# Kernel tuning notes

Hardware: AMD Instinct MI355X
Metric: run time of the kernel (lower is better)

The kernel has to match this reference:

```python
import jax, jax.numpy as jnp
import numpy as np

B, T, H = 16, 512, 384   # batch, phoneme length, hidden
F, K = 384, 3            # filter size, kernel size
DMAX = 8                 # max per-token duration
L = T * DMAX             # static max expanded length (original uses real_len.max())


def conv1d_same(x, w, b):
    # x: [B, T, Cin], w: [Cout, Cin, K] (torch OIW layout), padding = K//2 both sides
    y = jax.lax.conv_general_dilated(
        x.transpose(0, 2, 1), w, window_strides=(1,),
        padding=[(K // 2, K // 2)], dimension_numbers=('NCW', 'OIW', 'NCW'))
    return y.transpose(0, 2, 1) + b


def layer_norm(x, g, b, eps=1e-5):
    mu = jnp.mean(x, axis=-1, keepdims=True)
    var = jnp.mean(jnp.square(x - mu), axis=-1, keepdims=True)
    return (x - mu) * jax.lax.rsqrt(var + eps) * g + b


def setup_inputs() -> dict:
    key = jax.random.key(0)
    ks = jax.random.split(key, 10)
    x = jax.random.normal(ks[0], (B, T, H), dtype=jnp.float32)
    # log-durations whose exp().round() gives integers in [1, DMAX]
    dur = jax.random.randint(ks[1], (B, T), 1, DMAX + 1)
    true_durations = jnp.log(dur.astype(jnp.float32))
    s1 = 1.0 / np.sqrt(H * K)
    s2 = 1.0 / np.sqrt(F * K)
    s3 = 1.0 / np.sqrt(F)
    return {
        'x': x,
        'true_durations': true_durations,
        'conv1_w': jax.random.uniform(ks[2], (F, H, K), jnp.float32, -s1, s1),
        'conv1_b': jnp.zeros((F,), jnp.float32),
        'ln1_g': jnp.ones((F,), jnp.float32),
        'ln1_b': jnp.zeros((F,), jnp.float32),
        'conv2_w': jax.random.uniform(ks[3], (F, F, K), jnp.float32, -s2, s2),
        'conv2_b': jnp.zeros((F,), jnp.float32),
        'ln2_g': jnp.ones((F,), jnp.float32),
        'ln2_b': jnp.zeros((F,), jnp.float32),
        'lin_w': jax.random.uniform(ks[4], (F, 1), jnp.float32, -s3, s3),
        'lin_b': jnp.zeros((1,), jnp.float32),
    }


def reference(x, true_durations, conv1_w, conv1_b, ln1_g, ln1_b,
              conv2_w, conv2_b, ln2_g, ln2_b, lin_w, lin_b):
    # duration predictor net (dropout in eval mode = identity)
    h = conv1d_same(x, conv1_w, conv1_b)
    h = jax.nn.gelu(layer_norm(h, ln1_g, ln1_b), approximate=False)
    h = conv1d_same(h, conv2_w, conv2_b)
    h = jax.nn.gelu(layer_norm(h, ln2_g, ln2_b), approximate=False)
    length = jax.nn.relu(h @ lin_w + lin_b)[..., 0]  # [B, T]

    # length regulation with ground-truth durations (detached ints in original)
    dur = jnp.round(jnp.exp(true_durations)).astype(jnp.int32)  # [B, T]
    ends = jnp.cumsum(dur, axis=1)          # [B, T]
    starts = ends - dur                     # [B, T]
    k = jnp.arange(L)                       # [L]
    # binary alignment: A[b,t,l] = 1 iff starts[b,t] <= l < ends[b,t]
    A = ((k >= starts[..., None]) & (k < ends[..., None])).astype(x.dtype)  # [B,T,L]
    out = jnp.einsum('bth,btl->blh', x, A)  # = (x^T @ A)^T, [B, L, H]
    return out, length
```

## Files before the change

kernel.cpp:

```cpp
#include <hip/hip_runtime.h>
#include <stdint.h>

typedef unsigned short u16;
typedef unsigned int   u32;

#define B_    16
#define T_    512
#define H_    384
#define F_    384
#define DMAX_ 8
#define L_    4096
#define KD    1152
#define M_    8192

typedef __bf16 bf16x8 __attribute__((ext_vector_type(8)));
typedef float  f32x4  __attribute__((ext_vector_type(4)));

typedef __attribute__((address_space(1))) u32 gu32;
typedef __attribute__((address_space(3))) u32 lu32;

__device__ __forceinline__ void dma16(const void* g, void* l) {
    __builtin_amdgcn_global_load_lds((gu32*)(uintptr_t)g, (lu32*)(u32)(uintptr_t)l, 16, 0, 0);
}

__device__ __forceinline__ u16 f2b(float f) {
    union { float f; u32 i; } v; v.f = f;
    u32 x = v.i;
    return (u16)((x + 0x7fffu + ((x >> 16) & 1u)) >> 16);
}

__global__ void k_prep(const float* __restrict__ td, const float* __restrict__ w1,
                       const float* __restrict__ w2, const float* __restrict__ x,
                       int* __restrict__ tmap, u16* __restrict__ Wp1,
                       u16* __restrict__ Wp2, u16* __restrict__ xb,
                       u16* __restrict__ zp) {
    int blk = blockIdx.x, tid = threadIdx.x;
    if (blk < 16) {
        __shared__ int s[T_];
        int b = blk, t = tid;
        int d = (int)roundf(expf(td[b * T_ + t]));
        if (d < 0) d = 0; if (d > DMAX_) d = DMAX_;
        int v = d;
        s[t] = v;
        __syncthreads();
        for (int off = 1; off < T_; off <<= 1) {
            int add = (t >= off) ? s[t - off] : 0;
            __syncthreads();
            v += add;
            s[t] = v;
            __syncthreads();
        }
        int end = v, start = end - d;
        for (int i = start; i < end; ++i) tmap[b * L_ + i] = t;
        int total = s[T_ - 1];
        for (int l = total + t; l < L_; l += T_) tmap[b * L_ + l] = -1;
    } else if (blk == 16) {
        zp[tid] = 0;
    } else if (blk < 17 + 1728) {
        int j = (blk - 17) * 512 + tid;
        const int n = F_ * H_ * 3;
        const float* src = (j < n) ? w1 : w2;
        u16* dst         = (j < n) ? Wp1 : Wp2;
        int jj = (j < n) ? j : j - n;
        int f = jj / (H_ * 3);
        int rem = jj % (H_ * 3);
        int c = rem / 3, kk = rem % 3;
        dst[f * KD + kk * H_ + c] = f2b(src[jj]);
    } else {
        int v = (blk - 1745) * 512 + tid;
        float4 f = *(const float4*)(x + (size_t)v * 4);
        u16 o[4] = { f2b(f.x), f2b(f.y), f2b(f.z), f2b(f.w) };
        *(uint2*)(xb + (size_t)v * 4) = *(uint2*)o;
    }
}

__global__ void k_expand(const float* __restrict__ x, const int* __restrict__ tmap,
                         float* __restrict__ out) {
    int v = blockIdx.x * blockDim.x + threadIdx.x;
    if (v >= B_ * L_ * 96) return;
    int row = v / 96, c4 = v % 96;
    int b = row >> 12;
    int t = tmap[row];
    uint4 val = make_uint4(0u, 0u, 0u, 0u);
    if (t >= 0) val = *(const uint4*)(x + (size_t)((b << 9) + t) * H_ + c4 * 4);
    *(uint4*)(out + (size_t)row * H_ + c4 * 4) = val;
}

#define CH_ 3328

__device__ __forceinline__ void gemm_core(u16* smem, const u16* __restrict__ src,
                                          const u16* __restrict__ Wp,
                                          const u16* __restrict__ zp,
                                          int m0, int tid, f32x4 acc[2][3]) {
    int w = tid >> 6, lane = tid & 63;
    int quad = lane >> 4, l16 = lane & 15;

    const u16* bbase[6];
    int bdst[6];
    #pragma unroll
    for (int p = 0; p < 6; ++p) {
        int bc = p * 512 + tid;
        int rowB = bc >> 3;
        int qlB = (bc & 7) ^ (rowB & 7);
        bbase[p] = Wp + (size_t)rowB * KD + qlB * 8;
        bdst[p] = bc;
    }
    const u16* abase[3];
    int adst = 3072 + tid;
    {
        int rowA = (tid & 255) >> 3;
        int qlA = (tid & 7) ^ (rowA & 7);
        int arow = m0 + rowA;
        int bB = arow >> 9, tt = arow & 511;
        #pragma unroll
        for (int kk = 0; kk < 3; ++kk) {
            int ts = tt + kk - 1;
            abase[kk] = (ts >= 0 && ts < T_) ? (src + (size_t)((bB << 9) + ts) * H_ + qlA * 8)
                                             : (zp + qlA * 8);
        }
    }

    int aoff[2][2], boff[3][2];
    #pragma unroll
    for (int i = 0; i < 2; ++i)
        #pragma unroll
        for (int kv = 0; kv < 2; ++kv) {
            int row = i * 16 + l16;
            aoff[i][kv] = (3072 + ((row << 3) | ((kv * 4 + quad) ^ (row & 7)))) * 8;
        }
    #pragma unroll
    for (int j = 0; j < 3; ++j)
        #pragma unroll
        for (int kv = 0; kv < 2; ++kv) {
            int row = w * 48 + j * 16 + l16;
            boff[j][kv] = (((row << 3) | ((kv * 4 + quad) ^ (row & 7)))) * 8;
        }

    #pragma unroll
    for (int i = 0; i < 2; ++i)
        #pragma unroll
        for (int j = 0; j < 3; ++j)
            acc[i][j] = f32x4{0.f, 0.f, 0.f, 0.f};

    {
        u16* base = smem;
        #pragma unroll
        for (int p = 0; p < 6; ++p) dma16(bbase[p], base + (size_t)bdst[p] * 8);
        if (tid < 256) dma16(abase[0], base + (size_t)adst * 8);
    }

    int kk1 = 0, s61 = 0;
    for (int s = 0; s < 18; ++s) {
        __syncthreads();
        if (s < 17) {
            if (++s61 == 6) { s61 = 0; ++kk1; }
            int koff = (s + 1) * 64;
            u16* base = smem + (size_t)(((s + 1) & 1) ? CH_ : 0) * 8;
            #pragma unroll
            for (int p = 0; p < 6; ++p) dma16(bbase[p] + koff, base + (size_t)bdst[p] * 8);
            if (tid < 256) dma16(abase[kk1] + s61 * 64, base + (size_t)adst * 8);
        }
        const u16* rb = smem + (size_t)((s & 1) ? CH_ : 0) * 8;
        #pragma unroll
        for (int kv = 0; kv < 2; ++kv) {
            bf16x8 af0 = *(const bf16x8*)(rb + aoff[0][kv]);
            bf16x8 af1 = *(const bf16x8*)(rb + aoff[1][kv]);
            #pragma unroll
            for (int j = 0; j < 3; ++j) {
                bf16x8 bf = *(const bf16x8*)(rb + boff[j][kv]);
                acc[0][j] = __builtin_amdgcn_mfma_f32_16x16x32_bf16(af0, bf, acc[0][j], 0, 0, 0);
                acc[1][j] = __builtin_amdgcn_mfma_f32_16x16x32_bf16(af1, bf, acc[1][j], 0, 0, 0);
            }
        }
    }
    __syncthreads();
}

__launch_bounds__(512, 2)
__global__ void k_gemm1(const u16* __restrict__ xb, const u16* __restrict__ Wp,
                        const float* __restrict__ bias, const float* __restrict__ g,
                        const float* __restrict__ beta, u16* __restrict__ G,
                        const u16* __restrict__ zp) {
    __shared__ u16 smem[2 * CH_ * 8];
    int tid = threadIdx.x;
    int w = tid >> 6, lane = tid & 63;
    int quad = lane >> 4, l16 = lane & 15;
    int m0 = blockIdx.x * 32;

    f32x4 acc[2][3];
    gemm_core(smem, xb, Wp, zp, m0, tid, acc);

    float bcol[3], gcol[3], becol[3];
    #pragma unroll
    for (int j = 0; j < 3; ++j) {
        int col = w * 48 + j * 16 + l16;
        bcol[j] = bias[col]; gcol[j] = g[col]; becol[j] = beta[col];
    }
    float* sb  = (float*)smem;
    float* s2b = (float*)smem + 256;
    #pragma unroll
    for (int i = 0; i < 2; ++i)
        #pragma unroll
        for (int r = 0; r < 4; ++r) {
            float s = 0.f, s2 = 0.f;
            #pragma unroll
            for (int j = 0; j < 3; ++j) {
                float y = acc[i][j][r] + bcol[j];
                s += y; s2 += y * y;
            }
            #pragma unroll
            for (int off = 8; off; off >>= 1) { s += __shfl_down(s, off); s2 += __shfl_down(s2, off); }
            if (l16 == 0) {
                int rl = i * 16 + quad * 4 + r;
                sb[w * 32 + rl] = s; s2b[w * 32 + rl] = s2;
            }
        }
    __syncthreads();
    #pragma unroll
    for (int i = 0; i < 2; ++i)
        #pragma unroll
        for (int r = 0; r < 4; ++r) {
            int rl = i * 16 + quad * 4 + r;
            float S = 0.f, S2 = 0.f;
            #pragma unroll
            for (int w2 = 0; w2 < 8; ++w2) { S += sb[w2 * 32 + rl]; S2 += s2b[w2 * 32 + rl]; }
            float mean = S * (1.f / F_);
            float var  = S2 * (1.f / F_) - mean * mean;
            float rstd = rsqrtf(var + 1e-5f);
            #pragma unroll
            for (int j = 0; j < 3; ++j) {
                int col = w * 48 + j * 16 + l16;
                float y  = (acc[i][j][r] + bcol[j] - mean) * rstd * gcol[j] + becol[j];
                float gl = 0.5f * y * (1.f + erff(y * 0.70710678118654752f));
                G[(size_t)(m0 + rl) * F_ + col] = f2b(gl);
            }
        }
}

__launch_bounds__(512, 2)
__global__ void k_gemm2(const u16* __restrict__ G, const u16* __restrict__ Wp,
                        const float* __restrict__ bias, const float* __restrict__ g,
                        const float* __restrict__ beta, const float* __restrict__ lw,
                        const float* __restrict__ lb, float* __restrict__ out1,
                        const u16* __restrict__ zp) {
    __shared__ u16 smem[2 * CH_ * 8];
    int tid = threadIdx.x;
    int w = tid >> 6, lane = tid & 63;
    int quad = lane >> 4, l16 = lane & 15;
    int m0 = blockIdx.x * 32;

    f32x4 acc[2][3];
    gemm_core(smem, G, Wp, zp, m0, tid, acc);

    float bcol[3], gcol[3], becol[3], lwcol[3];
    #pragma unroll
    for (int j = 0; j < 3; ++j) {
        int col = w * 48 + j * 16 + l16;
        bcol[j] = bias[col]; gcol[j] = g[col]; becol[j] = beta[col]; lwcol[j] = lw[col];
    }
    float* sb  = (float*)smem;
    float* s2b = (float*)smem + 256;
    float* db  = (float*)smem + 512;
    #pragma unroll
    for (int i = 0; i < 2; ++i)
        #pragma unroll
        for (int r = 0; r < 4; ++r) {
            float s = 0.f, s2 = 0.f;
            #pragma unroll
            for (int j = 0; j < 3; ++j) {
                float y = acc[i][j][r] + bcol[j];
                s += y; s2 += y * y;
            }
            #pragma unroll
            for (int off = 8; off; off >>= 1) { s += __shfl_down(s, off); s2 += __shfl_down(s2, off); }
            if (l16 == 0) {
                int rl = i * 16 + quad * 4 + r;
                sb[w * 32 + rl] = s; s2b[w * 32 + rl] = s2;
            }
        }
    __syncthreads();
    #pragma unroll
    for (int i = 0; i < 2; ++i)
        #pragma unroll
        for (int r = 0; r < 4; ++r) {
            int rl = i * 16 + quad * 4 + r;
            float S = 0.f, S2 = 0.f;
            #pragma unroll
            for (int w2 = 0; w2 < 8; ++w2) { S += sb[w2 * 32 + rl]; S2 += s2b[w2 * 32 + rl]; }
            float mean = S * (1.f / F_);
            float var  = S2 * (1.f / F_) - mean * mean;
            float rstd = rsqrtf(var + 1e-5f);
            float dot = 0.f;
            #pragma unroll
            for (int j = 0; j < 3; ++j) {
                float y  = (acc[i][j][r] + bcol[j] - mean) * rstd * gcol[j] + becol[j];
                float gl = 0.5f * y * (1.f + erff(y * 0.70710678118654752f));
                dot += gl * lwcol[j];
            }
            #pragma unroll
            for (int off = 8; off; off >>= 1) dot += __shfl_down(dot, off);
            if (l16 == 0) db[w * 32 + rl] = dot;
        }
    __syncthreads();
    if (tid < 32) {
        float d = lb[0];
        #pragma unroll
        for (int w2 = 0; w2 < 8; ++w2) d += db[w2 * 32 + tid];
        out1[m0 + tid] = fmaxf(d, 0.f);
    }
}

extern "C" void kernel_launch(void* const* d_in, const int* in_sizes, int n_in,
                              void* d_out, int out_size, void* d_ws, size_t ws_size,
                              hipStream_t stream) {
    const float* x   = (const float*)d_in[0];
    const float* td  = (const float*)d_in[1];
    const float* w1  = (const float*)d_in[2];
    const float* b1  = (const float*)d_in[3];
    const float* g1  = (const float*)d_in[4];
    const float* be1 = (const float*)d_in[5];
    const float* w2  = (const float*)d_in[6];
    const float* b2  = (const float*)d_in[7];
    const float* g2  = (const float*)d_in[8];
    const float* be2 = (const float*)d_in[9];
    const float* lw  = (const float*)d_in[10];
    const float* lb  = (const float*)d_in[11];

    float* out0 = (float*)d_out;
    float* out1 = out0 + (size_t)B_ * L_ * H_;

    char* ws = (char*)d_ws;
    size_t off = 0;
    auto carve = [&](size_t bytes) -> void* {
        void* p = ws + off;
        off = (off + bytes + 255) & ~(size_t)255;
        return p;
    };
    int*  tmap = (int*)carve((size_t)B_ * L_ * sizeof(int));
    u16*  Wp1  = (u16*)carve((size_t)F_ * KD * sizeof(u16));
    u16*  Wp2  = (u16*)carve((size_t)F_ * KD * sizeof(u16));
    u16*  xb   = (u16*)carve((size_t)M_ * H_ * sizeof(u16));
    u16*  G    = (u16*)carve((size_t)M_ * F_ * sizeof(u16));
    u16*  zp   = (u16*)carve(1024);

    k_prep<<<3281, 512, 0, stream>>>(td, w1, w2, x, tmap, Wp1, Wp2, xb, zp);
    k_expand<<<(B_ * L_ * 96 + 255) / 256, 256, 0, stream>>>(x, tmap, out0);
    k_gemm1<<<M_ / 32, 512, 0, stream>>>(xb, Wp1, b1, g1, be1, G, zp);
    k_gemm2<<<M_ / 32, 512, 0, stream>>>(G, Wp2, b2, g2, be2, lw, lb, out1, zp);
}
```

Before: 187.3 us.

## Use 64-row GEMM tiles and fuse expand copy into conv1 kernel launch

The GEMM row tile grows from 32 to 64 rows with a 2x4 warp layout, so each block reuses the staged weight tile across twice as many rows. This halves the grid to 128 blocks per conv. The length-regulation expand copy is folded into the conv1 launch as extra blocks, so the memory-bound copy can overlap the GEMM and one launch goes away. The cost is larger LDS use and more accumulator registers, and with only 128 GEMM blocks the CUs may be underused. Conv2 in particular may lack parallelism.

Result: no change. 186.2 us (-0.6%).

```diff
diff --git a/kernel.cpp b/kernel.cpp
--- a/kernel.cpp
+++ b/kernel.cpp
@@ -74,79 +74,67 @@
     }
 }
 
-__global__ void k_expand(const float* __restrict__ x, const int* __restrict__ tmap,
-                         float* __restrict__ out) {
-    int v = blockIdx.x * blockDim.x + threadIdx.x;
-    if (v >= B_ * L_ * 96) return;
-    int row = v / 96, c4 = v % 96;
-    int b = row >> 12;
-    int t = tmap[row];
-    uint4 val = make_uint4(0u, 0u, 0u, 0u);
-    if (t >= 0) val = *(const uint4*)(x + (size_t)((b << 9) + t) * H_ + c4 * 4);
-    *(uint4*)(out + (size_t)row * H_ + c4 * 4) = val;
-}
-
-#define CH_ 3328
-
-__device__ __forceinline__ void gemm_core(u16* smem, const u16* __restrict__ src,
-                                          const u16* __restrict__ Wp,
-                                          const u16* __restrict__ zp,
-                                          int m0, int tid, f32x4 acc[2][3]) {
+#define CHT 3584
+#define DBO 28672
+
+__device__ __forceinline__ void gemm_core64(u16* smem, const u16* __restrict__ src,
+                                            const u16* __restrict__ Wp,
+                                            const u16* __restrict__ zp,
+                                            int m0, int tid, f32x4 acc[2][6]) {
     int w = tid >> 6, lane = tid & 63;
     int quad = lane >> 4, l16 = lane & 15;
-
+    int wm = w & 1, wn = w >> 1;
+
+    int rowA = tid >> 3;
+    int qlA  = (tid & 7) ^ (rowA & 7);
+    int arow = m0 + rowA;
+    int bB = arow >> 9, tt = arow & 511;
+    const u16* abase[3];
+    #pragma unroll
+    for (int kk = 0; kk < 3; ++kk) {
+        int ts = tt + kk - 1;
+        abase[kk] = (ts >= 0 && ts < T_) ? (src + (size_t)((bB << 9) + ts) * H_ + qlA * 8)
+                                         : (zp + qlA * 8);
+    }
+    int adst = tid * 8;
     const u16* bbase[6];
     int bdst[6];
     #pragma unroll
     for (int p = 0; p < 6; ++p) {
-        int bc = p * 512 + tid;
-        int rowB = bc >> 3;
-        int qlB = (bc & 7) ^ (rowB & 7);
+        int idx = p * 512 + tid;
+        int rowB = idx >> 3;
+        int qlB  = (tid & 7) ^ (rowB & 7);
         bbase[p] = Wp + (size_t)rowB * KD + qlB * 8;
-        bdst[p] = bc;
-    }
-    const u16* abase[3];
-    int adst = 3072 + tid;
-    {
-        int rowA = (tid & 255) >> 3;
-        int qlA = (tid & 7) ^ (rowA & 7);
-        int arow = m0 + rowA;
-        int bB = arow >> 9, tt = arow & 511;
-        #pragma unroll
-        for (int kk = 0; kk < 3; ++kk) {
-            int ts = tt + kk - 1;
-            abase[kk] = (ts >= 0 && ts < T_) ? (src + (size_t)((bB << 9) + ts) * H_ + qlA * 8)
-                                             : (zp + qlA * 8);
-        }
-    }
-
-    int aoff[2][2], boff[3][2];
+        bdst[p]  = (512 + idx) * 8;
+    }
+
+    int aoff[2][2], boff[6][2];
     #pragma unroll
     for (int i = 0; i < 2; ++i)
         #pragma unroll
         for (int kv = 0; kv < 2; ++kv) {
-            int row = i * 16 + l16;
-            aoff[i][kv] = (3072 + ((row << 3) | ((kv * 4 + quad) ^ (row & 7)))) * 8;
-        }
-    #pragma unroll
-    for (int j = 0; j < 3; ++j)
+            int row = wm * 32 + i * 16 + l16;
+            aoff[i][kv] = ((row << 3) | ((kv * 4 + quad) ^ (row & 7))) * 8;
+        }
+    #pragma unroll
+    for (int j = 0; j < 6; ++j)
         #pragma unroll
         for (int kv = 0; kv < 2; ++kv) {
-            int row = w * 48 + j * 16 + l16;
-            boff[j][kv] = (((row << 3) | ((kv * 4 + quad) ^ (row & 7)))) * 8;
-        }
-
-    #pragma unroll
-    for (int i = 0; i < 2; ++i)
-        #pragma unroll
-        for (int j = 0; j < 3; ++j)
+            int row = wn * 96 + j * 16 + l16;
+            boff[j][kv] = (512 + ((row << 3) | ((kv * 4 + quad) ^ (row & 7)))) * 8;
+        }
+
+    #pragma unroll
+    for (int i = 0; i < 2; ++i)
+        #pragma unroll
+        for (int j = 0; j < 6; ++j)
             acc[i][j] = f32x4{0.f, 0.f, 0.f, 0.f};
 
     {
         u16* base = smem;
         #pragma unroll
-        for (int p = 0; p < 6; ++p) dma16(bbase[p], base + (size_t)bdst[p] * 8);
-        if (tid < 256) dma16(abase[0], base + (size_t)adst * 8);
+        for (int p = 0; p < 6; ++p) dma16(bbase[p], base + bdst[p]);
+        dma16(abase[0], base + adst);
     }
 
     int kk1 = 0, s61 = 0;
@@ -155,18 +143,18 @@
         if (s < 17) {
             if (++s61 == 6) { s61 = 0; ++kk1; }
             int koff = (s + 1) * 64;
-            u16* base = smem + (size_t)(((s + 1) & 1) ? CH_ : 0) * 8;
-            #pragma unroll
-            for (int p = 0; p < 6; ++p) dma16(bbase[p] + koff, base + (size_t)bdst[p] * 8);
-            if (tid < 256) dma16(abase[kk1] + s61 * 64, base + (size_t)adst * 8);
-        }
-        const u16* rb = smem + (size_t)((s & 1) ? CH_ : 0) * 8;
+            u16* base = smem + (((s + 1) & 1) ? DBO : 0);
+            #pragma unroll
+            for (int p = 0; p < 6; ++p) dma16(bbase[p] + koff, base + bdst[p]);
+            dma16(abase[kk1] + s61 * 64, base + adst);
+        }
+        const u16* rb = smem + ((s & 1) ? DBO : 0);
         #pragma unroll
         for (int kv = 0; kv < 2; ++kv) {
             bf16x8 af0 = *(const bf16x8*)(rb + aoff[0][kv]);
             bf16x8 af1 = *(const bf16x8*)(rb + aoff[1][kv]);
             #pragma unroll
-            for (int j = 0; j < 3; ++j) {
+            for (int j = 0; j < 6; ++j) {
                 bf16x8 bf = *(const bf16x8*)(rb + boff[j][kv]);
                 acc[0][j] = __builtin_amdgcn_mfma_f32_16x16x32_bf16(af0, bf, acc[0][j], 0, 0, 0);
                 acc[1][j] = __builtin_amdgcn_mfma_f32_16x16x32_bf16(af1, bf, acc[1][j], 0, 0, 0);
@@ -176,24 +164,41 @@
     __syncthreads();
 }
 
-__launch_bounds__(512, 2)
-__global__ void k_gemm1(const u16* __restrict__ xb, const u16* __restrict__ Wp,
+__launch_bounds__(512)
+__global__ void k_main1(const u16* __restrict__ xb, const u16* __restrict__ Wp,
                         const float* __restrict__ bias, const float* __restrict__ g,
                         const float* __restrict__ beta, u16* __restrict__ G,
-                        const u16* __restrict__ zp) {
-    __shared__ u16 smem[2 * CH_ * 8];
+                        const u16* __restrict__ zp, const float* __restrict__ x,
+                        const int* __restrict__ tmap, float* __restrict__ out0) {
+    __shared__ u16 smem[2 * DBO];
     int tid = threadIdx.x;
+    if (blockIdx.x >= 128) {
+        int bi = blockIdx.x - 128;
+        int v0 = bi * 4096;
+        #pragma unroll
+        for (int it = 0; it < 8; ++it) {
+            int v = v0 + it * 512 + tid;
+            int row = v / 96, c4 = v % 96;
+            int b = row >> 12;
+            int t = tmap[row];
+            uint4 val = make_uint4(0u, 0u, 0u, 0u);
+            if (t >= 0) val = *(const uint4*)(x + (size_t)((b << 9) + t) * H_ + c4 * 4);
+            *(uint4*)(out0 + (size_t)row * H_ + c4 * 4) = val;
+        }
+        return;
+    }
     int w = tid >> 6, lane = tid & 63;
     int quad = lane >> 4, l16 = lane & 15;
-    int m0 = blockIdx.x * 32;
-
-    f32x4 acc[2][3];
-    gemm_core(smem, xb, Wp, zp, m0, tid, acc);
-
-    float bcol[3], gcol[3], becol[3];
-    #pragma unroll
-    for (int j = 0; j < 3; ++j) {
-        int col = w * 48 + j * 16 + l16;
+    int wm = w & 1, wn = w >> 1;
+    int m0 = blockIdx.x * 64;
+
+    f32x4 acc[2][6];
+    gemm_core64(smem, xb, Wp, zp, m0, tid, acc);
+
+    float bcol[6], gcol[6], becol[6];
+    #pragma unroll
+    for (int j = 0; j < 6; ++j) {
+        int col = wn * 96 + j * 16 + l16;
         bcol[j] = bias[col]; gcol[j] = g[col]; becol[j] = beta[col];
     }
     float* sb  = (float*)smem;
@@ -204,7 +209,7 @@
         for (int r = 0; r < 4; ++r) {
             float s = 0.f, s2 = 0.f;
             #pragma unroll
-            for (int j = 0; j < 3; ++j) {
+            for (int j = 0; j < 6; ++j) {
                 float y = acc[i][j][r] + bcol[j];
                 s += y; s2 += y * y;
             }
@@ -212,7 +217,7 @@
             for (int off = 8; off; off >>= 1) { s += __shfl_down(s, off); s2 += __shfl_down(s2, off); }
             if (l16 == 0) {
                 int rl = i * 16 + quad * 4 + r;
-                sb[w * 32 + rl] = s; s2b[w * 32 + rl] = s2;
+                sb[(wm * 4 + wn) * 32 + rl] = s; s2b[(wm * 4 + wn) * 32 + rl] = s2;
             }
         }
     __syncthreads();
@@ -223,39 +228,40 @@
             int rl = i * 16 + quad * 4 + r;
             float S = 0.f, S2 = 0.f;
             #pragma unroll
-            for (int w2 = 0; w2 < 8; ++w2) { S += sb[w2 * 32 + rl]; S2 += s2b[w2 * 32 + rl]; }
+            for (int p = 0; p < 4; ++p) { S += sb[(wm * 4 + p) * 32 + rl]; S2 += s2b[(wm * 4 + p) * 32 + rl]; }
             float mean = S * (1.f / F_);
             float var  = S2 * (1.f / F_) - mean * mean;
             float rstd = rsqrtf(var + 1e-5f);
             #pragma unroll
-            for (int j = 0; j < 3; ++j) {
-                int col = w * 48 + j * 16 + l16;
+            for (int j = 0; j < 6; ++j) {
+                int col = wn * 96 + j * 16 + l16;
                 float y  = (acc[i][j][r] + bcol[j] - mean) * rstd * gcol[j] + becol[j];
                 float gl = 0.5f * y * (1.f + erff(y * 0.70710678118654752f));
-                G[(size_t)(m0 + rl) * F_ + col] = f2b(gl);
-            }
-        }
-}
-
-__launch_bounds__(512, 2)
+                G[(size_t)(m0 + wm * 32 + rl) * F_ + col] = f2b(gl);
+            }
+        }
+}
+
+__launch_bounds__(512)
 __global__ void k_gemm2(const u16* __restrict__ G, const u16* __restrict__ Wp,
                         const float* __restrict__ bias, const float* __restrict__ g,
                         const float* __restrict__ beta, const float* __restrict__ lw,
                         const float* __restrict__ lb, float* __restrict__ out1,
                         const u16* __restrict__ zp) {
-    __shared__ u16 smem[2 * CH_ * 8];
+    __shared__ u16 smem[2 * DBO];
     int tid = threadIdx.x;
     int w = tid >> 6, lane = tid & 63;
     int quad = lane >> 4, l16 = lane & 15;
-    int m0 = blockIdx.x * 32;
-
-    f32x4 acc[2][3];
-    gemm_core(smem, G, Wp, zp, m0, tid, acc);
-
-    float bcol[3], gcol[3], becol[3], lwcol[3];
-    #pragma unroll
-    for (int j = 0; j < 3; ++j) {
-        int col = w * 48 + j * 16 + l16;
+    int wm = w & 1, wn = w >> 1;
+    int m0 = blockIdx.x * 64;
+
+    f32x4 acc[2][6];
+    gemm_core64(smem, G, Wp, zp, m0, tid, acc);
+
+    float bcol[6], gcol[6], becol[6], lwcol[6];
+    #pragma unroll
+    for (int j = 0; j < 6; ++j) {
+        int col = wn * 96 + j * 16 + l16;
         bcol[j] = bias[col]; gcol[j] = g[col]; becol[j] = beta[col]; lwcol[j] = lw[col];
     }
     float* sb  = (float*)smem;
@@ -267,7 +273,7 @@
         for (int r = 0; r < 4; ++r) {
             float s = 0.f, s2 = 0.f;
             #pragma unroll
-            for (int j = 0; j < 3; ++j) {
+            for (int j = 0; j < 6; ++j) {
                 float y = acc[i][j][r] + bcol[j];
                 s += y; s2 += y * y;
             }
@@ -275,7 +281,7 @@
             for (int off = 8; off; off >>= 1) { s += __shfl_down(s, off); s2 += __shfl_down(s2, off); }
             if (l16 == 0) {
                 int rl = i * 16 + quad * 4 + r;
-                sb[w * 32 + rl] = s; s2b[w * 32 + rl] = s2;
+                sb[(wm * 4 + wn) * 32 + rl] = s; s2b[(wm * 4 + wn) * 32 + rl] = s2;
             }
         }
     __syncthreads();
@@ -286,26 +292,27 @@
             int rl = i * 16 + quad * 4 + r;
             float S = 0.f, S2 = 0.f;
             #pragma unroll
-            for (int w2 = 0; w2 < 8; ++w2) { S += sb[w2 * 32 + rl]; S2 += s2b[w2 * 32 + rl]; }
+            for (int p = 0; p < 4; ++p) { S += sb[(wm * 4 + p) * 32 + rl]; S2 += s2b[(wm * 4 + p) * 32 + rl]; }
             float mean = S * (1.f / F_);
             float var  = S2 * (1.f / F_) - mean * mean;
             float rstd = rsqrtf(var + 1e-5f);
             float dot = 0.f;
             #pragma unroll
-            for (int j = 0; j < 3; ++j) {
+            for (int j = 0; j < 6; ++j) {
                 float y  = (acc[i][j][r] + bcol[j] - mean) * rstd * gcol[j] + becol[j];
                 float gl = 0.5f * y * (1.f + erff(y * 0.70710678118654752f));
                 dot += gl * lwcol[j];
             }
             #pragma unroll
             for (int off = 8; off; off >>= 1) dot += __shfl_down(dot, off);
-            if (l16 == 0) db[w * 32 + rl] = dot;
+            if (l16 == 0) db[(wm * 4 + wn) * 32 + rl] = dot;
         }
     __syncthreads();
-    if (tid < 32) {
+    if (tid < 64) {
+        int wmv = tid >> 5, rl = tid & 31;
         float d = lb[0];
         #pragma unroll
-        for (int w2 = 0; w2 < 8; ++w2) d += db[w2 * 32 + tid];
+        for (int p = 0; p < 4; ++p) d += db[(wmv * 4 + p) * 32 + rl];
         out1[m0 + tid] = fmaxf(d, 0.f);
     }
 }
@@ -344,7 +351,6 @@
     u16*  zp   = (u16*)carve(1024);
 
     k_prep<<<3281, 512, 0, stream>>>(td, w1, w2, x, tmap, Wp1, Wp2, xb, zp);
-    k_expand<<<(B_ * L_ * 96 + 255) / 256, 256, 0, stream>>>(x, tmap, out0);
-    k_gemm1<<<M_ / 32, 512, 0, stream>>>(xb, Wp1, b1, g1, be1, G, zp);
-    k_gemm2<<<M_ / 32, 512, 0, stream>>>(G, Wp2, b2, g2, be2, lw, lb, out1, zp);
-}
+    k_main1<<<128 + 1536, 512, 0, stream>>>(xb, Wp1, b1, g1, be1, G, zp, x, tmap, out0);
+    k_gemm2<<<128, 512, 0, stream>>>(G, Wp2, b2, g2, be2, lw, lb, out1, zp);
+}
```
